# Kernel optimization log

Hardware: AMD Instinct MI355X
Metric: run time of the kernel (lower is better)

The kernel has to match this reference:

```python
import jax, jax.numpy as jnp
import numpy as np

N_NODES = 50000
N_EDGES = 800000
IN_CH = 256
OUT_CH = 64
HEADS = 4
NEG_SLOPE = 0.2


def setup_inputs() -> dict:
    key = jax.random.key(0)
    k = jax.random.split(key, 7)
    x = jax.random.normal(k[0], (N_NODES, IN_CH), dtype=jnp.float32)
    edge_index = jax.random.randint(k[1], (2, N_EDGES), 0, N_NODES, dtype=jnp.int32)
    # Glorot-style init for the linear projection and attention vectors
    W = jax.random.normal(k[2], (IN_CH, HEADS * OUT_CH), dtype=jnp.float32) / np.sqrt(IN_CH)
    att_src = jax.random.normal(k[3], (HEADS, OUT_CH), dtype=jnp.float32) / np.sqrt(OUT_CH)
    att_dst = jax.random.normal(k[4], (HEADS, OUT_CH), dtype=jnp.float32) / np.sqrt(OUT_CH)
    bias = jnp.zeros((HEADS * OUT_CH,), dtype=jnp.float32)
    return {"x": x, "edge_index": edge_index, "W": W,
            "att_src": att_src, "att_dst": att_dst, "bias": bias}


def reference(x, edge_index, W, att_src, att_dst, bias):
    N = x.shape[0]
    # PyG GATConv default: add self-loops
    loop = jnp.arange(N, dtype=edge_index.dtype)
    src = jnp.concatenate([edge_index[0], loop])
    dst = jnp.concatenate([edge_index[1], loop])

    h = (x @ W).reshape(N, HEADS, OUT_CH)          # [N,H,C]
    a_src = jnp.einsum('nhc,hc->nh', h, att_src)    # [N,H]
    a_dst = jnp.einsum('nhc,hc->nh', h, att_dst)    # [N,H]

    alpha = a_src[src] + a_dst[dst]                 # [E,H]
    alpha = jax.nn.leaky_relu(alpha, NEG_SLOPE)

    # segment softmax over edges grouped by destination node
    amax = jax.ops.segment_max(alpha, dst, num_segments=N)
    amax = jnp.where(jnp.isfinite(amax), amax, 0.0)
    e = jnp.exp(alpha - amax[dst])
    denom = jax.ops.segment_sum(e, dst, num_segments=N)
    coef = e / (denom[dst] + 1e-16)                 # [E,H]

    msg = coef[..., None] * h[src]                  # [E,H,C]
    out = jax.ops.segment_sum(msg, dst, num_segments=N)  # [N,H,C]
    out = out.reshape(N, HEADS * OUT_CH) + bias
    return jax.nn.relu(out)
```

## Files before the change

kernel.cpp:

```cpp
#include <hip/hip_runtime.h>
#include <hip/hip_bf16.h>

#define HC 256
#define NEG_SLOPE 0.2f
#define BM 64
#define LDKF 264

typedef short short8_t __attribute__((ext_vector_type(8)));
typedef float float4_t __attribute__((ext_vector_type(4)));
typedef int   int4_t   __attribute__((ext_vector_type(4)));

__device__ __forceinline__ unsigned short f2bf(float f) {
  unsigned u = __float_as_uint(f);
  return (unsigned short)((u + 0x7fffu + ((u >> 16) & 1u)) >> 16);
}
__device__ __forceinline__ float bf2f(unsigned short b) {
  return __uint_as_float(((unsigned)b) << 16);
}

__global__ void wt_kernel(const float* __restrict__ W, unsigned short* __restrict__ Wt,
                          int* __restrict__ deg, int n)
{
  const int k = blockIdx.x;
  const int t = threadIdx.x;
  Wt[t * 256 + k] = f2bf(W[k * 256 + t]);
  const int i = k * 256 + t;
  if (i < n) deg[i] = 0;
}

__global__ __launch_bounds__(256) void gemm_deg(
    const float* __restrict__ x, const unsigned short* __restrict__ Wt,
    const float* __restrict__ att_src, const float* __restrict__ att_dst,
    unsigned short* __restrict__ h, float* __restrict__ a_src,
    float* __restrict__ a_dst, int nnodes,
    const int* __restrict__ ei, int* __restrict__ deg, int E, int NG, int ND)
{
  __shared__ unsigned short As[BM * LDKF];
  const int t = threadIdx.x;

  if (blockIdx.x >= NG) {
    const int b = blockIdx.x - NG;
    for (int e = b * 256 + t; e < E; e += ND * 256)
      atomicAdd(&deg[ei[E + e]], 1);
    return;
  }

  const int wv   = t >> 6;
  const int lane = t & 63;
  const int r0   = blockIdx.x * BM;

  {
    const int row = t >> 2, kcb = (t & 3) * 16;
    const int gr = r0 + row;
    #pragma unroll
    for (int k0 = 0; k0 < 256; k0 += 64) {
      float4 xv[4];
      if (gr < nnodes) {
        const float4* p = (const float4*)(x + (size_t)gr * 256 + k0 + kcb);
        xv[0] = p[0]; xv[1] = p[1]; xv[2] = p[2]; xv[3] = p[3];
      } else {
        xv[0] = xv[1] = xv[2] = xv[3] = make_float4(0.f, 0.f, 0.f, 0.f);
      }
      const float* f = (const float*)xv;
      unsigned pk[8];
      #pragma unroll
      for (int i = 0; i < 8; ++i) {
        __hip_bfloat162 b2 = __float22bfloat162_rn(make_float2(f[2 * i], f[2 * i + 1]));
        pk[i] = *(unsigned*)&b2;
      }
      uint4* d = (uint4*)&As[row * LDKF + k0 + kcb];
      d[0] = make_uint4(pk[0], pk[1], pk[2], pk[3]);
      d[1] = make_uint4(pk[4], pk[5], pk[6], pk[7]);
    }
  }
  __syncthreads();

  const int l15 = lane & 15, q = lane >> 4;
  float4_t acc[4][4] = {};

  const unsigned short* __restrict__ Bp = Wt + ((size_t)(64 * wv + l15)) * 256 + q * 8;

  #pragma unroll
  for (int kstep = 0; kstep < 8; ++kstep) {
    const int ko = kstep * 32;
    short8_t bfr[4], af[4];
    #pragma unroll
    for (int nt = 0; nt < 4; ++nt)
      bfr[nt] = *(const short8_t*)(Bp + nt * 16 * 256 + ko);
    #pragma unroll
    for (int mt = 0; mt < 4; ++mt)
      af[mt] = *(const short8_t*)&As[(16 * mt + l15) * LDKF + ko + q * 8];
    #pragma unroll
    for (int mt = 0; mt < 4; ++mt)
      #pragma unroll
      for (int nt = 0; nt < 4; ++nt)
        acc[mt][nt] = __builtin_amdgcn_mfma_f32_16x16x32_bf16(
            af[mt], bfr[nt], acc[mt][nt], 0, 0, 0);
  }

  float atts[4], attd[4];
  #pragma unroll
  for (int nt = 0; nt < 4; ++nt) {
    atts[nt] = att_src[wv * 64 + 16 * nt + l15];
    attd[nt] = att_dst[wv * 64 + 16 * nt + l15];
  }

  #pragma unroll
  for (int mt = 0; mt < 4; ++mt) {
    #pragma unroll
    for (int reg = 0; reg < 4; ++reg) {
      const int row = r0 + 16 * mt + 4 * q + reg;
      const bool ok = row < nnodes;
      float ps = 0.f, pd = 0.f;
      #pragma unroll
      for (int nt = 0; nt < 4; ++nt) {
        const float v = acc[mt][nt][reg];
        if (ok) h[(size_t)row * 256 + 64 * wv + 16 * nt + l15] = f2bf(v);
        ps += v * atts[nt];
        pd += v * attd[nt];
      }
      #pragma unroll
      for (int off = 8; off; off >>= 1) {
        ps += __shfl_down(ps, off, 16);
        pd += __shfl_down(pd, off, 16);
      }
      if (ok && l15 == 0) {
        a_src[row * 4 + wv] = ps;
        a_dst[row * 4 + wv] = pd;
      }
    }
  }
}

__global__ __launch_bounds__(256) void scan_p1(const int* __restrict__ deg,
                                               int* __restrict__ bsum, int n)
{
  __shared__ int ws[4];
  const int t = threadIdx.x, lane = t & 63, wv = t >> 6;
  const int base = blockIdx.x * 1024 + t * 4;
  int4 v = make_int4(0, 0, 0, 0);
  if (base + 3 < n) v = *(const int4*)&deg[base];
  else {
    if (base + 0 < n) v.x = deg[base + 0];
    if (base + 1 < n) v.y = deg[base + 1];
    if (base + 2 < n) v.z = deg[base + 2];
  }
  int s = (v.x + v.y) + (v.z + v.w);
  #pragma unroll
  for (int off = 32; off; off >>= 1) s += __shfl_down(s, off, 64);
  if (lane == 0) ws[wv] = s;
  __syncthreads();
  if (t == 0) bsum[blockIdx.x] = (ws[0] + ws[1]) + (ws[2] + ws[3]);
}

__global__ __launch_bounds__(1024) void scan_p2(const int* __restrict__ bsum,
                                                int* __restrict__ boff,
                                                int* __restrict__ rowptr,
                                                int nb, int n)
{
  __shared__ int wsum[16], woff[16];
  const int t = threadIdx.x, lane = t & 63, wv = t >> 6;
  int v = (t < nb) ? bsum[t] : 0;
  int sc = v;
  #pragma unroll
  for (int off = 1; off < 64; off <<= 1) {
    int u = __shfl_up(sc, off, 64);
    if (lane >= off) sc += u;
  }
  if (lane == 63) wsum[wv] = sc;
  __syncthreads();
  if (t == 0) {
    int run = 0;
    #pragma unroll
    for (int i = 0; i < 16; ++i) { int x = wsum[i]; woff[i] = run; run += x; }
    rowptr[n] = run;
  }
  __syncthreads();
  if (t < nb) boff[t] = woff[wv] + sc - v;
}

__global__ __launch_bounds__(256) void scan_p3(const int* __restrict__ deg,
                                               const int* __restrict__ boff,
                                               int* __restrict__ rowptr,
                                               int* __restrict__ cursor, int n)
{
  __shared__ int wsum[4], woff[4];
  const int t = threadIdx.x, lane = t & 63, wv = t >> 6;
  const int base = blockIdx.x * 1024 + t * 4;
  int4 v = make_int4(0, 0, 0, 0);
  if (base + 3 < n) v = *(const int4*)&deg[base];
  else {
    if (base + 0 < n) v.x = deg[base + 0];
    if (base + 1 < n) v.y = deg[base + 1];
    if (base + 2 < n) v.z = deg[base + 2];
  }
  const int s = (v.x + v.y) + (v.z + v.w);
  int sc = s;
  #pragma unroll
  for (int off = 1; off < 64; off <<= 1) {
    int u = __shfl_up(sc, off, 64);
    if (lane >= off) sc += u;
  }
  if (lane == 63) wsum[wv] = sc;
  __syncthreads();
  if (t == 0) {
    int run = 0;
    #pragma unroll
    for (int i = 0; i < 4; ++i) { int x = wsum[i]; woff[i] = run; run += x; }
  }
  __syncthreads();
  int excl = boff[blockIdx.x] + woff[wv] + (sc - s);
  int4 r;
  r.x = excl;
  r.y = r.x + v.x;
  r.z = r.y + v.y;
  r.w = r.z + v.z;
  if (base + 3 < n) {
    *(int4*)&rowptr[base] = r;
    *(int4*)&cursor[base] = r;
  } else {
    if (base + 0 < n) { rowptr[base + 0] = r.x; cursor[base + 0] = r.x; }
    if (base + 1 < n) { rowptr[base + 1] = r.y; cursor[base + 1] = r.y; }
    if (base + 2 < n) { rowptr[base + 2] = r.z; cursor[base + 2] = r.z; }
  }
}

__global__ __launch_bounds__(256) void fill_csr(
    const int* __restrict__ ei, int* __restrict__ cursor,
    int* __restrict__ csr_src, int E, int nnodes)
{
  const int g    = blockIdx.x & 7;
  const int bg   = blockIdx.x >> 3;
  const int nbg  = gridDim.x >> 3;
  const int gsz  = (nnodes + 7) >> 3;
  const int dlo  = g * gsz;
  const int dhi  = min(dlo + gsz, nnodes);

  for (int e = bg * 256 + threadIdx.x; e < E; e += nbg * 256) {
    const int d = ei[E + e];
    if (d < dlo || d >= dhi) continue;
    const int pos = atomicAdd(&cursor[d], 1);
    csr_src[pos] = ei[e];
  }
}

__device__ __forceinline__ float4 ld_h(const unsigned short* __restrict__ h,
                                       int row, int cb)
{
  const ushort4 u = *(const ushort4*)&h[(size_t)row * 256 + cb];
  return make_float4(bf2f(u.x), bf2f(u.y), bf2f(u.z), bf2f(u.w));
}

__device__ __forceinline__ float edge_w(float as, float ad)
{
  float al = as + ad;
  al = al > 0.f ? al : NEG_SLOPE * al;
  return expf(al);
}

__global__ __launch_bounds__(256) void gather_kernel(
    const int* __restrict__ rowptr, const int* __restrict__ csr_src,
    const unsigned short* __restrict__ h,
    const float* __restrict__ a_src, const float* __restrict__ a_dst,
    const float* __restrict__ bias, float* __restrict__ out, int d0, int dend)
{
  const int wave = threadIdx.x >> 6;
  const int lane = threadIdx.x & 63;
  const int d = d0 + blockIdx.x * 4 + wave;
  if (d >= dend) return;

  const int head = lane >> 4;
  const int cb   = lane * 4;

  const float ad = a_dst[d * 4 + head];

  const float w = edge_w(a_src[d * 4 + head], ad);
  float dsum = w;
  float4 hv = ld_h(h, d, cb);
  float4 acc = make_float4(w * hv.x, w * hv.y, w * hv.z, w * hv.w);

  int j = rowptr[d];
  const int end = rowptr[d + 1];

  int4_t sC = {0, 0, 0, 0};
  if (j + 3 < end)
    sC = __builtin_nontemporal_load((const int4_t*)&csr_src[j]);
  while (j + 3 < end) {
    const int jn = j + 4;
    const int jp = (jn + 3 < end) ? jn : j;
    const int4_t sN = __builtin_nontemporal_load((const int4_t*)&csr_src[jp]);

    const float as0 = a_src[sC.x * 4 + head];
    const float as1 = a_src[sC.y * 4 + head];
    const float as2 = a_src[sC.z * 4 + head];
    const float as3 = a_src[sC.w * 4 + head];
    const float4 h0 = ld_h(h, sC.x, cb);
    const float4 h1 = ld_h(h, sC.y, cb);
    const float4 h2 = ld_h(h, sC.z, cb);
    const float4 h3 = ld_h(h, sC.w, cb);

    const float w0 = edge_w(as0, ad);
    const float w1 = edge_w(as1, ad);
    const float w2 = edge_w(as2, ad);
    const float w3 = edge_w(as3, ad);

    dsum += (w0 + w1) + (w2 + w3);
    acc.x += w0 * h0.x + w1 * h1.x + w2 * h2.x + w3 * h3.x;
    acc.y += w0 * h0.y + w1 * h1.y + w2 * h2.y + w3 * h3.y;
    acc.z += w0 * h0.z + w1 * h1.z + w2 * h2.z + w3 * h3.z;
    acc.w += w0 * h0.w + w1 * h1.w + w2 * h2.w + w3 * h3.w;

    sC = sN; j = jn;
  }
  for (; j < end; ++j) {
    const int s0 = csr_src[j];
    const float w0 = edge_w(a_src[s0 * 4 + head], ad);
    const float4 h0 = ld_h(h, s0, cb);
    dsum += w0;
    acc.x += w0 * h0.x; acc.y += w0 * h0.y;
    acc.z += w0 * h0.z; acc.w += w0 * h0.w;
  }

  const float inv = 1.f / (dsum + 1e-16f);
  const float4 b4 = ((const float4*)bias)[lane];
  float4 o;
  o.x = acc.x * inv + b4.x; o.x = o.x > 0.f ? o.x : 0.f;
  o.y = acc.y * inv + b4.y; o.y = o.y > 0.f ? o.y : 0.f;
  o.z = acc.z * inv + b4.z; o.z = o.z > 0.f ? o.z : 0.f;
  o.w = acc.w * inv + b4.w; o.w = o.w > 0.f ? o.w : 0.f;
  *(float4*)&out[(size_t)d * 256 + cb] = o;
}

extern "C" void kernel_launch(void* const* d_in, const int* in_sizes, int n_in,
                              void* d_out, int out_size, void* d_ws, size_t ws_size,
                              hipStream_t stream)
{
  const float* x       = (const float*)d_in[0];
  const int*   ei      = (const int*)d_in[1];
  const float* W       = (const float*)d_in[2];
  const float* att_src = (const float*)d_in[3];
  const float* att_dst = (const float*)d_in[4];
  const float* bias    = (const float*)d_in[5];

  const int nnodes = in_sizes[0] / HC;
  const int E      = in_sizes[1] / 2;
  const int nb     = (nnodes + 1023) / 1024;

  float* out = (float*)d_out;
  char* ws = (char*)d_ws;
  unsigned short* h  = (unsigned short*)ws;
  float* a_src = (float*)(ws + (size_t)nnodes * HC * 2);
  float* a_dst = a_src + (size_t)nnodes * 4;
  unsigned short* Wt = (unsigned short*)(a_dst + (size_t)nnodes * 4);
  int* deg    = (int*)((char*)Wt + 256 * 256 * 2);
  int* rowptr = deg + nnodes;
  int* cursor = rowptr + ((nnodes + 1 + 3) & ~3);
  int* bsum   = cursor + nnodes;
  int* boff   = bsum + ((nb + 3) & ~3);
  int* csr    = boff + ((nb + 3) & ~3);

  const int NG = (nnodes + BM - 1) / BM;
  const int ND = 1024;

  wt_kernel<<<256, 256, 0, stream>>>(W, Wt, deg, nnodes);

  gemm_deg<<<NG + ND, 256, 0, stream>>>(
      x, Wt, att_src, att_dst, h, a_src, a_dst, nnodes, ei, deg, E, NG, ND);

  scan_p1<<<nb, 256, 0, stream>>>(deg, bsum, nnodes);
  scan_p2<<<1, 1024, 0, stream>>>(bsum, boff, rowptr, nb, nnodes);
  scan_p3<<<nb, 256, 0, stream>>>(deg, boff, rowptr, cursor, nnodes);

  fill_csr<<<1024, 256, 0, stream>>>(ei, cursor, csr, E, nnodes);

  const int qn = (nnodes + 3) / 4;
  for (int qi = 0; qi < 4; ++qi) {
    const int d0   = qi * qn;
    const int dend = min(d0 + qn, nnodes);
    const int nblk = (dend - d0 + 3) / 4;
    if (nblk > 0)
      gather_kernel<<<nblk, 256, 0, stream>>>(
          rowptr, csr, h, a_src, a_dst, bias, out, d0, dend);
  }
}
```

Baseline: 289.9 us.

## Prepack W in MFMA fragment order, transpose GEMM output, single gather launch

The weight preprocessing now packs W into bf16 in the exact per-lane MFMA fragment order, so each B-operand load is a contiguous 16-byte per-lane read. The MFMA operands are swapped so each lane holds four consecutive output columns of one node. That allows packed 8-byte bf16 stores of h and a shorter cross-lane reduction for the attention logits. The four chunked gather launches are merged into one launch to cut launch overhead, which also removes the chunking's possible cache-locality benefit.

New measurement: 258.9 us. 10.7% less time.

```diff
diff --git a/kernel.cpp b/kernel.cpp
--- a/kernel.cpp
+++ b/kernel.cpp
@@ -18,18 +18,32 @@
   return __uint_as_float(((unsigned)b) << 16);
 }
 
-__global__ void wt_kernel(const float* __restrict__ W, unsigned short* __restrict__ Wt,
-                          int* __restrict__ deg, int n)
-{
-  const int k = blockIdx.x;
-  const int t = threadIdx.x;
-  Wt[t * 256 + k] = f2bf(W[k * 256 + t]);
-  const int i = k * 256 + t;
-  if (i < n) deg[i] = 0;
+__global__ __launch_bounds__(256) void wq_kernel(
+    const float* __restrict__ W, unsigned short* __restrict__ Wq,
+    int* __restrict__ deg, int n)
+{
+  const int f = blockIdx.x * 256 + threadIdx.x;
+  if (f < 8192) {
+    const int wv    = f >> 11;
+    const int nt    = (f >> 9) & 3;
+    const int kstep = (f >> 6) & 7;
+    const int l     = f & 63;
+    const int ncol  = 64 * wv + 16 * nt + (l & 15);
+    const int k0    = kstep * 32 + (l >> 4) * 8;
+    unsigned pk[4];
+    #pragma unroll
+    for (int i = 0; i < 4; ++i) {
+      __hip_bfloat162 b2 = __float22bfloat162_rn(make_float2(
+          W[(k0 + 2 * i) * 256 + ncol], W[(k0 + 2 * i + 1) * 256 + ncol]));
+      pk[i] = *(unsigned*)&b2;
+    }
+    *(uint4*)&Wq[(size_t)f * 8] = make_uint4(pk[0], pk[1], pk[2], pk[3]);
+  }
+  if (f < n) deg[f] = 0;
 }
 
 __global__ __launch_bounds__(256) void gemm_deg(
-    const float* __restrict__ x, const unsigned short* __restrict__ Wt,
+    const float* __restrict__ x, const unsigned short* __restrict__ Wq,
     const float* __restrict__ att_src, const float* __restrict__ att_dst,
     unsigned short* __restrict__ h, float* __restrict__ a_src,
     float* __restrict__ a_dst, int nnodes,
@@ -78,7 +92,7 @@
   const int l15 = lane & 15, q = lane >> 4;
   float4_t acc[4][4] = {};
 
-  const unsigned short* __restrict__ Bp = Wt + ((size_t)(64 * wv + l15)) * 256 + q * 8;
+  const unsigned short* __restrict__ Bq = Wq + (size_t)wv * 16384 + lane * 8;
 
   #pragma unroll
   for (int kstep = 0; kstep < 8; ++kstep) {
@@ -86,7 +100,7 @@
     short8_t bfr[4], af[4];
     #pragma unroll
     for (int nt = 0; nt < 4; ++nt)
-      bfr[nt] = *(const short8_t*)(Bp + nt * 16 * 256 + ko);
+      bfr[nt] = *(const short8_t*)(Bq + nt * 4096 + kstep * 512);
     #pragma unroll
     for (int mt = 0; mt < 4; ++mt)
       af[mt] = *(const short8_t*)&As[(16 * mt + l15) * LDKF + ko + q * 8];
@@ -95,39 +109,38 @@
       #pragma unroll
       for (int nt = 0; nt < 4; ++nt)
         acc[mt][nt] = __builtin_amdgcn_mfma_f32_16x16x32_bf16(
-            af[mt], bfr[nt], acc[mt][nt], 0, 0, 0);
-  }
-
-  float atts[4], attd[4];
+            bfr[nt], af[mt], acc[mt][nt], 0, 0, 0);
+  }
+
+  float4 as4[4], ad4[4];
   #pragma unroll
   for (int nt = 0; nt < 4; ++nt) {
-    atts[nt] = att_src[wv * 64 + 16 * nt + l15];
-    attd[nt] = att_dst[wv * 64 + 16 * nt + l15];
+    as4[nt] = *(const float4*)&att_src[64 * wv + 16 * nt + 4 * q];
+    ad4[nt] = *(const float4*)&att_dst[64 * wv + 16 * nt + 4 * q];
   }
 
   #pragma unroll
   for (int mt = 0; mt < 4; ++mt) {
-    #pragma unroll
-    for (int reg = 0; reg < 4; ++reg) {
-      const int row = r0 + 16 * mt + 4 * q + reg;
-      const bool ok = row < nnodes;
-      float ps = 0.f, pd = 0.f;
-      #pragma unroll
-      for (int nt = 0; nt < 4; ++nt) {
-        const float v = acc[mt][nt][reg];
-        if (ok) h[(size_t)row * 256 + 64 * wv + 16 * nt + l15] = f2bf(v);
-        ps += v * atts[nt];
-        pd += v * attd[nt];
+    const int node = r0 + 16 * mt + l15;
+    const bool ok = node < nnodes;
+    float ps = 0.f, pd = 0.f;
+    #pragma unroll
+    for (int nt = 0; nt < 4; ++nt) {
+      const float4_t v = acc[mt][nt];
+      if (ok) {
+        __hip_bfloat162 b01 = __float22bfloat162_rn(make_float2(v[0], v[1]));
+        __hip_bfloat162 b23 = __float22bfloat162_rn(make_float2(v[2], v[3]));
+        uint2 u = make_uint2(*(unsigned*)&b01, *(unsigned*)&b23);
+        *(uint2*)&h[(size_t)node * 256 + 64 * wv + 16 * nt + 4 * q] = u;
       }
-      #pragma unroll
-      for (int off = 8; off; off >>= 1) {
-        ps += __shfl_down(ps, off, 16);
-        pd += __shfl_down(pd, off, 16);
-      }
-      if (ok && l15 == 0) {
-        a_src[row * 4 + wv] = ps;
-        a_dst[row * 4 + wv] = pd;
-      }
+      ps += v[0] * as4[nt].x + v[1] * as4[nt].y + v[2] * as4[nt].z + v[3] * as4[nt].w;
+      pd += v[0] * ad4[nt].x + v[1] * ad4[nt].y + v[2] * ad4[nt].z + v[3] * ad4[nt].w;
+    }
+    ps += __shfl_down(ps, 16); ps += __shfl_down(ps, 32);
+    pd += __shfl_down(pd, 16); pd += __shfl_down(pd, 32);
+    if (ok && lane < 16) {
+      a_src[node * 4 + wv] = ps;
+      a_dst[node * 4 + wv] = pd;
     }
   }
 }
@@ -262,12 +275,12 @@
     const int* __restrict__ rowptr, const int* __restrict__ csr_src,
     const unsigned short* __restrict__ h,
     const float* __restrict__ a_src, const float* __restrict__ a_dst,
-    const float* __restrict__ bias, float* __restrict__ out, int d0, int dend)
+    const float* __restrict__ bias, float* __restrict__ out, int n)
 {
   const int wave = threadIdx.x >> 6;
   const int lane = threadIdx.x & 63;
-  const int d = d0 + blockIdx.x * 4 + wave;
-  if (d >= dend) return;
+  const int d = blockIdx.x * 4 + wave;
+  if (d >= n) return;
 
   const int head = lane >> 4;
   const int cb   = lane * 4;
@@ -351,8 +364,8 @@
   unsigned short* h  = (unsigned short*)ws;
   float* a_src = (float*)(ws + (size_t)nnodes * HC * 2);
   float* a_dst = a_src + (size_t)nnodes * 4;
-  unsigned short* Wt = (unsigned short*)(a_dst + (size_t)nnodes * 4);
-  int* deg    = (int*)((char*)Wt + 256 * 256 * 2);
+  unsigned short* Wq = (unsigned short*)(a_dst + (size_t)nnodes * 4);
+  int* deg    = (int*)((char*)Wq + 256 * 256 * 2);
   int* rowptr = deg + nnodes;
   int* cursor = rowptr + ((nnodes + 1 + 3) & ~3);
   int* bsum   = cursor + nnodes;
@@ -362,10 +375,10 @@
   const int NG = (nnodes + BM - 1) / BM;
   const int ND = 1024;
 
-  wt_kernel<<<256, 256, 0, stream>>>(W, Wt, deg, nnodes);
+  wq_kernel<<<256, 256, 0, stream>>>(W, Wq, deg, nnodes);
 
   gemm_deg<<<NG + ND, 256, 0, stream>>>(
-      x, Wt, att_src, att_dst, h, a_src, a_dst, nnodes, ei, deg, E, NG, ND);
+      x, Wq, att_src, att_dst, h, a_src, a_dst, nnodes, ei, deg, E, NG, ND);
 
   scan_p1<<<nb, 256, 0, stream>>>(deg, bsum, nnodes);
   scan_p2<<<1, 1024, 0, stream>>>(bsum, boff, rowptr, nb, nnodes);
@@ -373,13 +386,6 @@
 
   fill_csr<<<1024, 256, 0, stream>>>(ei, cursor, csr, E, nnodes);
 
-  const int qn = (nnodes + 3) / 4;
-  for (int qi = 0; qi < 4; ++qi) {
-    const int d0   = qi * qn;
-    const int dend = min(d0 + qn, nnodes);
-    const int nblk = (dend - d0 + 3) / 4;
-    if (nblk > 0)
-      gather_kernel<<<nblk, 256, 0, stream>>>(
-          rowptr, csr, h, a_src, a_dst, bias, out, d0, dend);
-  }
-}
+  gather_kernel<<<(nnodes + 3) / 4, 256, 0, stream>>>(
+      rowptr, csr, h, a_src, a_dst, bias, out, nnodes);
+}
```
